# Kernel tuning notes

Hardware: AMD Instinct MI355X
Metric: run time of the kernel (lower is better)

Reference implementation:

```python
import jax, jax.numpy as jnp
import numpy as np

FC = 2048      # fc_feat_size
VEMB = 512     # video_embedding_size
WEMB = 512     # word_embedding_size
H = 512        # lstm_hidden_size
A = 256        # att_hidden_size
TV = 32        # video_time_step
TC = 20        # caption_time_step
BC = 16        # batch_size_caption
RP = 32        # rp_num (proposals per caption)
B = BC * RP    # batch_size
GLOVE = 300


def setup_inputs() -> dict:
    key = jax.random.key(0)
    ks = jax.random.split(key, 12)
    def u(k, shape):
        return jax.random.uniform(k, shape, jnp.float32, -0.1, 0.1)
    def n(k, shape, s=0.05):
        return jax.random.normal(k, shape, jnp.float32) * s
    return {
        "video_fc_feat": jax.random.normal(ks[0], (B, TV, FC), jnp.float32),
        "video_caption": jax.random.normal(ks[1], (BC, TC, GLOVE), jnp.float32),
        "cap_length_list": jax.random.randint(ks[2], (BC,), 0, TC),
        # video_embedding / word_embedding (Linear layers)
        "W_vemb": u(ks[3], (VEMB, FC)), "b_vemb": jnp.zeros((VEMB,), jnp.float32),
        "W_wemb": u(ks[4], (WEMB, GLOVE)), "b_wemb": jnp.zeros((WEMB,), jnp.float32),
        # LSTMCell for video (gate order i,f,g,o as in torch)
        "Wih_v": n(ks[5], (4 * H, VEMB)), "Whh_v": n(ks[6], (4 * H, H)),
        "bih_v": jnp.zeros((4 * H,), jnp.float32), "bhh_v": jnp.zeros((4 * H,), jnp.float32),
        # LSTMCell for caption
        "Wih_c": n(ks[7], (4 * H, WEMB)), "Whh_c": n(ks[8], (4 * H, H)),
        "bih_c": jnp.zeros((4 * H,), jnp.float32), "bhh_c": jnp.zeros((4 * H,), jnp.float32),
        # attention linears
        "W_vid": u(ks[9], (A, H)), "b_vid": jnp.zeros((A,), jnp.float32),
        "W_sen": u(ks[10], (A, H)), "b_sen": jnp.zeros((A,), jnp.float32),
        "W_att": u(ks[11], (1, A)), "b_att": jnp.zeros((1,), jnp.float32),
    }


def _lstm(x_seq, Wih, Whh, bih, bhh):
    # x_seq: [B, T, D] -> hidden states [B, T, H]; torch LSTMCell gate order i,f,g,o
    Bb = x_seq.shape[0]
    Hh = Whh.shape[1]
    def step(carry, x):
        h, c = carry
        g = x @ Wih.T + bih + h @ Whh.T + bhh
        i, f, gg, o = jnp.split(g, 4, axis=-1)
        c = jax.nn.sigmoid(f) * c + jax.nn.sigmoid(i) * jnp.tanh(gg)
        h = jax.nn.sigmoid(o) * jnp.tanh(c)
        return (h, c), h
    init = (jnp.zeros((Bb, Hh), x_seq.dtype), jnp.zeros((Bb, Hh), x_seq.dtype))
    _, hs = jax.lax.scan(step, init, jnp.swapaxes(x_seq, 0, 1))
    return jnp.swapaxes(hs, 0, 1)


def reference(video_fc_feat, video_caption, cap_length_list,
              W_vemb, b_vemb, W_wemb, b_wemb,
              Wih_v, Whh_v, bih_v, bhh_v,
              Wih_c, Whh_c, bih_c, bhh_c,
              W_vid, b_vid, W_sen, b_sen, W_att, b_att):
    Bb, TVv, _ = video_fc_feat.shape
    BCc, TCc, _ = video_caption.shape
    rp = Bb // BCc
    Hh = Whh_v.shape[1]

    # caption LSTM over embedded GloVe words
    cap_x = video_caption @ W_wemb.T + b_wemb                 # [BC, TC, WEMB]
    cap_h = _lstm(cap_x, Wih_c, Whh_c, bih_c, bhh_c)          # [BC, TC, H]
    # video LSTM over embedded fc features
    vid_x = video_fc_feat @ W_vemb.T + b_vemb                 # [B, TV, VEMB]
    vid_h = _lstm(vid_x, Wih_v, Whh_v, bih_v, bhh_v)          # [B, TV, H]

    # additive attention: tanh(vid_linear(h_v) + sen_linear(h_c)) -> att_linear
    c_lin = cap_h @ W_sen.T + b_sen                           # [BC, TC, A]
    v_lin = (vid_h @ W_vid.T + b_vid).reshape(BCc, rp, TVv, -1)  # [BC, RP, TV, A]
    scores = (jnp.tanh(v_lin[:, :, :, None, :] + c_lin[:, None, None, :, :])
              @ W_att.T + b_att)[..., 0]                      # [BC, RP, TV, TC]

    # ragged masked softmax over caption length (max(len, 1) as in original)
    cap_len = jnp.maximum(cap_length_list, 1)
    mask = jnp.arange(TCc)[None, :] < cap_len[:, None]        # [BC, TC]
    m = mask[:, None, None, :]
    w = jax.nn.softmax(jnp.where(m, scores, -1e9), axis=-1)
    w = jnp.where(m, w, 0.0)                                  # [BC, RP, TV, TC]

    att_cap = jnp.einsum('brvt,bth->brvh', w, cap_h)          # [BC, RP, TV, H]
    cap_ftr_mean = att_cap.mean(axis=2)                       # mean over video steps
    vid_mean = vid_h.mean(axis=1).reshape(BCc, rp, Hh)
    return (vid_mean, cap_ftr_mean)
```

## Files before the change

### kernel.cpp

```cpp
#include <hip/hip_runtime.h>
#include <hip/hip_bf16.h>

#define FCD 2048
#define VEMBD 512
#define WEMBD 512
#define HD 512
#define AD 256
#define TVD 32
#define TCD 20
#define BCD 16
#define RPD 32
#define BD 512
#define GLOVED 300

typedef __attribute__((ext_vector_type(8))) short short8v;
typedef __attribute__((ext_vector_type(4))) float f32x4;

__device__ __forceinline__ float sigf(float x) { return 1.0f / (1.0f + __expf(-x)); }
__device__ __forceinline__ float tanhfast(float x) {
    float e = __expf(2.0f * x);
    return 1.0f - 2.0f / (e + 1.0f);
}
__device__ __forceinline__ unsigned short f2bf(float x) {
    union { __hip_bfloat16 h; unsigned short u; } v;
    v.h = __float2bfloat16(x);
    return v.u;
}
__device__ __forceinline__ float b2f(unsigned short u) {
    union { unsigned int i; float f; } v;
    v.i = ((unsigned int)u) << 16;
    return v.f;
}

__launch_bounds__(256)
__global__ void conv_f2b_kernel(const float* __restrict__ src,
                                unsigned short* __restrict__ dst, int n4) {
    for (int i = blockIdx.x * 256 + threadIdx.x; i < n4; i += gridDim.x * 256) {
        const float4 v = ((const float4*)src)[i];
        ushort4 o;
        o.x = f2bf(v.x); o.y = f2bf(v.y); o.z = f2bf(v.z); o.w = f2bf(v.w);
        ((ushort4*)dst)[i] = o;
    }
}

__launch_bounds__(256)
__global__ void conv_wcat_perm_kernel(const float* __restrict__ Wih,
                                      const float* __restrict__ Whh,
                                      unsigned short* __restrict__ Wcat) {
    const int gp = blockIdx.x;
    const int q = (gp >> 4) & 3;
    const int hc = (gp >> 6) * 16 + (gp & 15);
    const long g = (long)(q * 512 + hc);
    for (int k = threadIdx.x; k < 512; k += 256) {
        Wcat[(long)gp * 1024 + k]       = f2bf(Wih[g * 512 + k]);
        Wcat[(long)gp * 1024 + 512 + k] = f2bf(Whh[g * 512 + k]);
    }
}

__launch_bounds__(256)
__global__ void conv_bsum_kernel(const float* __restrict__ bih,
                                 const float* __restrict__ bhh,
                                 float* __restrict__ bsum) {
    const int gp = blockIdx.x * 256 + threadIdx.x;
    if (gp < 2048) {
        const int q = (gp >> 4) & 3;
        const int hc = (gp >> 6) * 16 + (gp & 15);
        const int g = q * 512 + hc;
        bsum[gp] = bih[g] + bhh[g];
    }
}

template<int AF32, int OBF>
__launch_bounds__(256)
__global__ void mfma_gemm128(const void* __restrict__ A,
                             const unsigned short* __restrict__ Bw,
                             const float* __restrict__ bias,
                             void* __restrict__ Cout,
                             int M, int N, int K)
{
    __shared__ unsigned short As[128][72];
    __shared__ unsigned short Bs[128][72];
    const int m0 = blockIdx.x * 128;
    const int n0 = blockIdx.y * 128;
    const int tid = threadIdx.x;
    const int lane = tid & 63;
    const int wid = tid >> 6;
    const int wm = (wid >> 1) * 64;
    const int wn = (wid & 1) * 64;
    const int lrow = lane & 15;
    const int lko = (lane >> 4) * 8;
    const int sr = tid >> 1;
    const int sc = (tid & 1) * 32;

    f32x4 acc[4][4] = {};

    const float* Arow_f = (const float*)A + (long)(m0 + sr) * K;
    const unsigned short* Arow_b = (const unsigned short*)A + (long)(m0 + sr) * K;
    const unsigned short* Brow = Bw + (long)(n0 + sr) * K;

    if (AF32) {
#pragma unroll
        for (int i = 0; i < 8; i++) {
            const float4 v = *(const float4*)(Arow_f + sc + i * 4);
            unsigned short* d = &As[sr][sc + i * 4];
            d[0] = f2bf(v.x); d[1] = f2bf(v.y); d[2] = f2bf(v.z); d[3] = f2bf(v.w);
        }
    } else {
#pragma unroll
        for (int i = 0; i < 4; i++)
            *(short8v*)&As[sr][sc + i * 8] = *(const short8v*)(Arow_b + sc + i * 8);
    }
#pragma unroll
    for (int i = 0; i < 4; i++)
        *(short8v*)&Bs[sr][sc + i * 8] = *(const short8v*)(Brow + sc + i * 8);
    __syncthreads();

    const int nc = K >> 6;
    float4 paf[8];
    short8v pab[4], pb[4];
    for (int c = 0; c < nc; c++) {
        if (c < nc - 1) {
            const int k0 = (c + 1) * 64;
            if (AF32) {
#pragma unroll
                for (int i = 0; i < 8; i++)
                    paf[i] = *(const float4*)(Arow_f + k0 + sc + i * 4);
            } else {
#pragma unroll
                for (int i = 0; i < 4; i++)
                    pab[i] = *(const short8v*)(Arow_b + k0 + sc + i * 8);
            }
#pragma unroll
            for (int i = 0; i < 4; i++)
                pb[i] = *(const short8v*)(Brow + k0 + sc + i * 8);
        }
#pragma unroll
        for (int kk = 0; kk < 2; kk++) {
            short8v a[4], b[4];
#pragma unroll
            for (int mi = 0; mi < 4; mi++)
                a[mi] = *(const short8v*)&As[wm + mi * 16 + lrow][kk * 32 + lko];
#pragma unroll
            for (int ni = 0; ni < 4; ni++)
                b[ni] = *(const short8v*)&Bs[wn + ni * 16 + lrow][kk * 32 + lko];
#pragma unroll
            for (int mi = 0; mi < 4; mi++)
#pragma unroll
                for (int ni = 0; ni < 4; ni++)
                    acc[mi][ni] = __builtin_amdgcn_mfma_f32_16x16x32_bf16(
                        a[mi], b[ni], acc[mi][ni], 0, 0, 0);
        }
        __syncthreads();
        if (c < nc - 1) {
            if (AF32) {
#pragma unroll
                for (int i = 0; i < 8; i++) {
                    unsigned short* d = &As[sr][sc + i * 4];
                    d[0] = f2bf(paf[i].x); d[1] = f2bf(paf[i].y);
                    d[2] = f2bf(paf[i].z); d[3] = f2bf(paf[i].w);
                }
            } else {
#pragma unroll
                for (int i = 0; i < 4; i++)
                    *(short8v*)&As[sr][sc + i * 8] = pab[i];
            }
#pragma unroll
            for (int i = 0; i < 4; i++)
                *(short8v*)&Bs[sr][sc + i * 8] = pb[i];
            __syncthreads();
        }
    }

    const int rbase = (lane >> 4) * 4;
#pragma unroll
    for (int ni = 0; ni < 4; ni++) {
        const int col = n0 + wn + ni * 16 + lrow;
        const float bv = bias[col];
#pragma unroll
        for (int mi = 0; mi < 4; mi++) {
#pragma unroll
            for (int j = 0; j < 4; j++) {
                const long row = m0 + wm + mi * 16 + rbase + j;
                const float val = acc[mi][ni][j] + bv;
                if (OBF) ((unsigned short*)Cout)[row * N + col] = f2bf(val);
                else     ((float*)Cout)[row * N + col] = val;
            }
        }
    }
}

__launch_bounds__(256, 2)
__global__ void step_fused(const unsigned short* __restrict__ vx,
                           const unsigned short* __restrict__ h_in,
                           unsigned short* __restrict__ h_out,
                           const unsigned short* __restrict__ Wcat,
                           const float* __restrict__ bsum,
                           float* __restrict__ c_state,
                           unsigned short* __restrict__ vid_h,
                           int t,
                           const float* __restrict__ xg,
                           const float* __restrict__ Whh_c,
                           const float* __restrict__ bhh_c,
                           const float* __restrict__ hc_in,
                           float* __restrict__ hc_out,
                           float* __restrict__ cap_cst,
                           float* __restrict__ cap_h)
{
    __shared__ __align__(16) unsigned char smem[26112];
    const int bx = blockIdx.x;
    const int tid = threadIdx.x;

    if (bx >= 512) {
        const int h0 = (bx - 512) * 16;
        float* Wsc = (float*)smem;
        float* Hshc = (float*)(smem + 17408);
        const int tx = tid & 15;
        const int ty = tid >> 4;
        const int lrow2 = tid >> 2;
        const int lq = tid & 3;
        float acc4[4] = {};

        for (int k0 = 0; k0 < 512; k0 += 64) {
            {
                const int q = lrow2 >> 4;
                const int hcc = lrow2 & 15;
                const float* src = Whh_c + (long)(q * 512 + h0 + hcc) * 512 + k0 + lq * 16;
                const int col = hcc * 4 + q;
#pragma unroll
                for (int j = 0; j < 4; j++) {
                    const float4 v = *(const float4*)(src + j * 4);
                    Wsc[(lq * 16 + j * 4 + 0) * 68 + col] = v.x;
                    Wsc[(lq * 16 + j * 4 + 1) * 68 + col] = v.y;
                    Wsc[(lq * 16 + j * 4 + 2) * 68 + col] = v.z;
                    Wsc[(lq * 16 + j * 4 + 3) * 68 + col] = v.w;
                }
            }
            {
                const int lb = tid >> 4;
                const int lk4 = (tid & 15) * 4;
                *(float4*)&Hshc[lb * 68 + lk4] = *(const float4*)(hc_in + (long)lb * 512 + k0 + lk4);
            }
            __syncthreads();
#pragma unroll
            for (int kq = 0; kq < 16; kq++) {
                const float4 h4 = *(const float4*)&Hshc[ty * 68 + kq * 4];
                const float4 w0 = *(const float4*)&Wsc[(kq * 4 + 0) * 68 + tx * 4];
                const float4 w1 = *(const float4*)&Wsc[(kq * 4 + 1) * 68 + tx * 4];
                const float4 w2 = *(const float4*)&Wsc[(kq * 4 + 2) * 68 + tx * 4];
                const float4 w3 = *(const float4*)&Wsc[(kq * 4 + 3) * 68 + tx * 4];
                acc4[0] += h4.x * w0.x + h4.y * w1.x + h4.z * w2.x + h4.w * w3.x;
                acc4[1] += h4.x * w0.y + h4.y * w1.y + h4.z * w2.y + h4.w * w3.y;
                acc4[2] += h4.x * w0.z + h4.y * w1.z + h4.z * w2.z + h4.w * w3.z;
                acc4[3] += h4.x * w0.w + h4.y * w1.w + h4.z * w2.w + h4.w * w3.w;
            }
            __syncthreads();
        }
        const int hc = h0 + tx;
        const long xrow = (long)(ty * TCD + t) * 2048;
        const float gi = acc4[0] + xg[xrow + hc]        + bhh_c[hc];
        const float gf = acc4[1] + xg[xrow + 512 + hc]  + bhh_c[512 + hc];
        const float gg = acc4[2] + xg[xrow + 1024 + hc] + bhh_c[1024 + hc];
        const float go = acc4[3] + xg[xrow + 1536 + hc] + bhh_c[1536 + hc];
        const float c_old = cap_cst[(long)ty * 512 + hc];
        const float ii = sigf(gi), ff = sigf(gf), g2 = tanhfast(gg), oo = sigf(go);
        const float c = ff * c_old + ii * g2;
        const float h = oo * tanhfast(c);
        cap_cst[(long)ty * 512 + hc] = c;
        hc_out[(long)ty * 512 + hc] = h;
        cap_h[(long)(ty * TCD + t) * 512 + hc] = h;
        return;
    }

    const int n0 = (bx & 31) * 64;
    const int b0 = (bx >> 5) * 32;
    const int lane = tid & 63;
    const int w = tid >> 6;
    const int bi = w & 1;
    const int nq = w >> 1;
    const int lrow = lane & 15;
    const int lko = (lane >> 4) * 8;
    const int sra = tid >> 3;
    const int sca = (tid & 7) * 16;

    unsigned short* As = (unsigned short*)smem;
    unsigned short* Ws = (unsigned short*)(smem + 8704);

    const unsigned short* arow_vx = vx + ((long)(b0 + sra) * TVD + t) * 512;
    const unsigned short* arow_h  = h_in + (long)(b0 + sra) * 512;
    const unsigned short* wrow0   = Wcat + (long)(n0 + sra) * 1024;
    const unsigned short* wrow1   = Wcat + (long)(n0 + sra + 32) * 1024;

    f32x4 acc[2] = {};

    *(short8v*)&As[sra * 136 + sca]     = *(const short8v*)(arow_vx + sca);
    *(short8v*)&As[sra * 136 + sca + 8] = *(const short8v*)(arow_vx + sca + 8);
    *(short8v*)&Ws[sra * 136 + sca]            = *(const short8v*)(wrow0 + sca);
    *(short8v*)&Ws[sra * 136 + sca + 8]        = *(const short8v*)(wrow0 + sca + 8);
    *(short8v*)&Ws[(sra + 32) * 136 + sca]     = *(const short8v*)(wrow1 + sca);
    *(short8v*)&Ws[(sra + 32) * 136 + sca + 8] = *(const short8v*)(wrow1 + sca + 8);
    __syncthreads();

    short8v pa0, pa1, pw0, pw1, pw2, pw3;
    for (int c = 0; c < 8; c++) {
        if (c < 7) {
            const int k0 = (c + 1) * 128;
            const unsigned short* ap = (k0 < 512) ? (arow_vx + k0) : (arow_h + (k0 - 512));
            pa0 = *(const short8v*)(ap + sca);
            pa1 = *(const short8v*)(ap + sca + 8);
            pw0 = *(const short8v*)(wrow0 + k0 + sca);
            pw1 = *(const short8v*)(wrow0 + k0 + sca + 8);
            pw2 = *(const short8v*)(wrow1 + k0 + sca);
            pw3 = *(const short8v*)(wrow1 + k0 + sca + 8);
        }
#pragma unroll
        for (int kk = 0; kk < 4; kk++) {
            const short8v a = *(const short8v*)&As[(bi * 16 + lrow) * 136 + kk * 32 + lko];
#pragma unroll
            for (int nl = 0; nl < 2; nl++) {
                const short8v b = *(const short8v*)&Ws[((nq * 2 + nl) * 16 + lrow) * 136 + kk * 32 + lko];
                acc[nl] = __builtin_amdgcn_mfma_f32_16x16x32_bf16(a, b, acc[nl], 0, 0, 0);
            }
        }
        __syncthreads();
        if (c < 7) {
            *(short8v*)&As[sra * 136 + sca]            = pa0;
            *(short8v*)&As[sra * 136 + sca + 8]        = pa1;
            *(short8v*)&Ws[sra * 136 + sca]            = pw0;
            *(short8v*)&Ws[sra * 136 + sca + 8]        = pw1;
            *(short8v*)&Ws[(sra + 32) * 136 + sca]     = pw2;
            *(short8v*)&Ws[(sra + 32) * 136 + sca + 8] = pw3;
            __syncthreads();
        }
    }

    float* red = (float*)smem;
    const int rbase = (lane >> 4) * 4;
    if (w >= 2) {
#pragma unroll
        for (int nl = 0; nl < 2; nl++)
#pragma unroll
            for (int j = 0; j < 4; j++)
                red[nl * 512 + (bi * 16 + rbase + j) * 16 + lrow] = acc[nl][j];
    }
    __syncthreads();
    if (w < 2) {
        const int hc = (n0 >> 2) + lrow;
        const float bs0 = bsum[n0 + lrow];
        const float bs1 = bsum[n0 + 16 + lrow];
        const float bs2 = bsum[n0 + 32 + lrow];
        const float bs3 = bsum[n0 + 48 + lrow];
#pragma unroll
        for (int j = 0; j < 4; j++) {
            const int blocal = bi * 16 + rbase + j;
            const long b = b0 + blocal;
            const float gi = acc[0][j] + bs0;
            const float gf = acc[1][j] + bs1;
            const float gg = red[blocal * 16 + lrow] + bs2;
            const float go = red[512 + blocal * 16 + lrow] + bs3;
            const float c_old = c_state[b * 512 + hc];
            const float ii = sigf(gi), ff = sigf(gf), g2 = tanhfast(gg), oo = sigf(go);
            const float cn = ff * c_old + ii * g2;
            const float h = oo * tanhfast(cn);
            c_state[b * 512 + hc] = cn;
            h_out[b * 512 + hc] = f2bf(h);
            vid_h[(b * TVD + t) * 512 + hc] = f2bf(h);
        }
    }
}

__launch_bounds__(256)
__global__ void gemm_bias_kernel(const float* __restrict__ A,
                                 const float* __restrict__ Bw,
                                 const float* __restrict__ bias,
                                 float* __restrict__ C,
                                 int M, int N, int K) {
    __shared__ float As[16][68];
    __shared__ float Bs[16][68];
    const int n0 = blockIdx.x * 64;
    const int m0 = blockIdx.y * 64;
    const int tid = threadIdx.x;
    const int tx = tid & 15;
    const int ty = tid >> 4;
    const int lrow = tid >> 2;
    const int lk4 = (tid & 3) * 4;

    float acc[4][4] = {};

    for (int k0 = 0; k0 < K; k0 += 16) {
        {
            const float* src = A + (long)(m0 + lrow) * K + k0 + lk4;
            float4 v;
            if (k0 + 16 <= K) v = *(const float4*)src;
            else {
                v.x = (k0 + lk4 + 0 < K) ? src[0] : 0.f;
                v.y = (k0 + lk4 + 1 < K) ? src[1] : 0.f;
                v.z = (k0 + lk4 + 2 < K) ? src[2] : 0.f;
                v.w = (k0 + lk4 + 3 < K) ? src[3] : 0.f;
            }
            As[lk4 + 0][lrow] = v.x; As[lk4 + 1][lrow] = v.y;
            As[lk4 + 2][lrow] = v.z; As[lk4 + 3][lrow] = v.w;
        }
        {
            const float* src = Bw + (long)(n0 + lrow) * K + k0 + lk4;
            float4 v;
            if (k0 + 16 <= K) v = *(const float4*)src;
            else {
                v.x = (k0 + lk4 + 0 < K) ? src[0] : 0.f;
                v.y = (k0 + lk4 + 1 < K) ? src[1] : 0.f;
                v.z = (k0 + lk4 + 2 < K) ? src[2] : 0.f;
                v.w = (k0 + lk4 + 3 < K) ? src[3] : 0.f;
            }
            Bs[lk4 + 0][lrow] = v.x; Bs[lk4 + 1][lrow] = v.y;
            Bs[lk4 + 2][lrow] = v.z; Bs[lk4 + 3][lrow] = v.w;
        }
        __syncthreads();
#pragma unroll
        for (int kk = 0; kk < 16; kk++) {
            const float4 av = *(const float4*)&As[kk][ty * 4];
            const float4 bv = *(const float4*)&Bs[kk][tx * 4];
            acc[0][0] += av.x * bv.x; acc[0][1] += av.x * bv.y; acc[0][2] += av.x * bv.z; acc[0][3] += av.x * bv.w;
            acc[1][0] += av.y * bv.x; acc[1][1] += av.y * bv.y; acc[1][2] += av.y * bv.z; acc[1][3] += av.y * bv.w;
            acc[2][0] += av.z * bv.x; acc[2][1] += av.z * bv.y; acc[2][2] += av.z * bv.z; acc[2][3] += av.z * bv.w;
            acc[3][0] += av.w * bv.x; acc[3][1] += av.w * bv.y; acc[3][2] += av.w * bv.z; acc[3][3] += av.w * bv.w;
        }
        __syncthreads();
    }

    const float b0v = bias[n0 + tx * 4 + 0];
    const float b1v = bias[n0 + tx * 4 + 1];
    const float b2v = bias[n0 + tx * 4 + 2];
    const float b3v = bias[n0 + tx * 4 + 3];
#pragma unroll
    for (int i = 0; i < 4; i++) {
        float* dst = C + (long)(m0 + ty * 4 + i) * N + n0 + tx * 4;
        dst[0] = acc[i][0] + b0v;
        dst[1] = acc[i][1] + b1v;
        dst[2] = acc[i][2] + b2v;
        dst[3] = acc[i][3] + b3v;
    }
}

__launch_bounds__(256)
__global__ void attn_kernel(const float* __restrict__ v_lin,
                            const float* __restrict__ c_lin,
                            const float* __restrict__ W_att,
                            const float* __restrict__ b_att,
                            const int* __restrict__ cap_len,
                            const float* __restrict__ cap_h,
                            float* __restrict__ out2)
{
    const int br = blockIdx.x;
    const int bc = br >> 5;
    const int tid = threadIdx.x;
    const int lane = tid & 63;
    const int wv = tid >> 6;
    __shared__ float cl[TCD][AD];
    __shared__ float vl[AD];
    __shared__ float sl[TVD][TCD];
    __shared__ float wsum[TCD];

    for (int tt = 0; tt < TCD; tt++)
        cl[tt][tid] = c_lin[(long)(bc * TCD + tt) * AD + tid];
    const float wa0 = W_att[lane];
    const float wa1 = W_att[64 + lane];
    const float wa2 = W_att[128 + lane];
    const float wa3 = W_att[192 + lane];
    const float batt = b_att[0];
    __syncthreads();

    for (int v = 0; v < TVD; v++) {
        vl[tid] = v_lin[((long)br * TVD + v) * AD + tid];
        __syncthreads();
        const float v0 = vl[lane], v1 = vl[64 + lane], v2 = vl[128 + lane], v3 = vl[192 + lane];
#pragma unroll
        for (int dt = 0; dt < 5; dt++) {
            const int t = wv * 5 + dt;
            float s = tanhfast(v0 + cl[t][lane]) * wa0
                    + tanhfast(v1 + cl[t][64 + lane]) * wa1
                    + tanhfast(v2 + cl[t][128 + lane]) * wa2
                    + tanhfast(v3 + cl[t][192 + lane]) * wa3;
            for (int off = 32; off > 0; off >>= 1) s += __shfl_down(s, off, 64);
            if (lane == 0) sl[v][t] = s + batt;
        }
        __syncthreads();
    }

    int L = cap_len[bc];
    if (L < 1) L = 1;
    if (tid < TVD) {
        const int v = tid;
        float m = -1e30f;
        for (int t = 0; t < TCD; t++)
            if (t < L) m = fmaxf(m, sl[v][t]);
        float sum = 0.f;
        for (int t = 0; t < TCD; t++)
            if (t < L) sum += __expf(sl[v][t] - m);
        const float inv = 1.f / sum;
        for (int t = 0; t < TCD; t++)
            sl[v][t] = (t < L) ? __expf(sl[v][t] - m) * inv : 0.f;
    }
    __syncthreads();
    if (tid < TCD) {
        float s = 0.f;
        for (int v = 0; v < TVD; v++) s += sl[v][tid];
        wsum[tid] = s * (1.0f / TVD);
    }
    __syncthreads();

    const float* chb = cap_h + (long)bc * TCD * HD;
#pragma unroll
    for (int r = 0; r < 2; r++) {
        const int h = r * 256 + tid;
        float s = 0.f;
#pragma unroll
        for (int t = 0; t < TCD; t++)
            s += wsum[t] * chb[t * HD + h];
        out2[(long)br * HD + h] = s;
    }
}

__launch_bounds__(256)
__global__ void vidmean_bf_kernel(const unsigned short* __restrict__ vid_h,
                                  float* __restrict__ out1)
{
    const int idx = blockIdx.x * 256 + threadIdx.x;
    const int b = idx >> 6;
    const int h8 = (idx & 63) * 8;
    float s[8] = {};
    for (int t = 0; t < TVD; t++) {
        const short8v v = *(const short8v*)(vid_h + ((long)b * TVD + t) * 512 + h8);
#pragma unroll
        for (int j = 0; j < 8; j++) s[j] += b2f((unsigned short)v[j]);
    }
#pragma unroll
    for (int j = 0; j < 8; j++)
        out1[(long)b * 512 + h8 + j] = s[j] * (1.0f / TVD);
}

extern "C" void kernel_launch(void* const* d_in, const int* in_sizes, int n_in,
                              void* d_out, int out_size, void* d_ws, size_t ws_size,
                              hipStream_t stream) {
    const float* video_fc      = (const float*)d_in[0];
    const float* video_caption = (const float*)d_in[1];
    const int*   cap_len       = (const int*)d_in[2];
    const float* W_vemb = (const float*)d_in[3];
    const float* b_vemb = (const float*)d_in[4];
    const float* W_wemb = (const float*)d_in[5];
    const float* b_wemb = (const float*)d_in[6];
    const float* Wih_v  = (const float*)d_in[7];
    const float* Whh_v  = (const float*)d_in[8];
    const float* bih_v  = (const float*)d_in[9];
    const float* bhh_v  = (const float*)d_in[10];
    const float* Wih_c  = (const float*)d_in[11];
    const float* Whh_c  = (const float*)d_in[12];
    const float* bih_c  = (const float*)d_in[13];
    const float* bhh_c  = (const float*)d_in[14];
    const float* W_vid  = (const float*)d_in[15];
    const float* b_vid  = (const float*)d_in[16];
    const float* W_sen  = (const float*)d_in[17];
    const float* b_sen  = (const float*)d_in[18];
    const float* W_att  = (const float*)d_in[19];
    const float* b_att  = (const float*)d_in[20];

    float* out1 = (float*)d_out;
    float* out2 = out1 + BD * HD;

    float* ws = (float*)d_ws;
    size_t off = 0;
    auto alloc = [&](size_t nfloats) {
        float* p = ws + off;
        off += (nfloats + 63) & ~(size_t)63;
        return p;
    };
    unsigned short* vidx_bf = (unsigned short*)alloc((size_t)BD * TVD * VEMBD / 2);
    unsigned short* vidh_bf = (unsigned short*)alloc((size_t)BD * TVD * HD / 2);
    unsigned short* h_bf_a  = (unsigned short*)alloc((size_t)BD * HD / 2);
    unsigned short* h_bf_b  = (unsigned short*)alloc((size_t)BD * HD / 2);
    float* c_st    = alloc((size_t)BD * HD);
    float* v_lin   = alloc((size_t)BD * TVD * AD);
    unsigned short* Wvemb_bf = (unsigned short*)alloc((size_t)VEMBD * FCD / 2);
    unsigned short* Wvid_bf  = (unsigned short*)alloc((size_t)AD * HD / 2);
    unsigned short* Wcat_bf  = (unsigned short*)alloc((size_t)2048 * 1024 / 2);
    float* bsum    = alloc(2048);
    float* cap_x   = alloc((size_t)BCD * TCD * WEMBD);
    float* xg_c    = alloc((size_t)BCD * TCD * 4 * HD);
    float* cap_h   = alloc((size_t)BCD * TCD * HD);
    float* c_lin   = alloc((size_t)BCD * TCD * AD);
    float* cap_ha  = alloc((size_t)BCD * HD);
    float* cap_hb  = alloc((size_t)BCD * HD);
    float* cap_cst = alloc((size_t)BCD * HD);
    const size_t fcn = (size_t)BD * TVD * FCD;
    const bool preconv = ((off + fcn / 2 + 64) * sizeof(float) <= ws_size);
    unsigned short* vidfc_bf = preconv ? (unsigned short*)alloc(fcn / 2) : nullptr;

    hipMemsetAsync(h_bf_a, 0, (size_t)BD * HD * sizeof(unsigned short), stream);
    hipMemsetAsync(c_st, 0, (size_t)BD * HD * sizeof(float), stream);
    hipMemsetAsync(cap_ha, 0, (size_t)BCD * HD * sizeof(float), stream);
    hipMemsetAsync(cap_cst, 0, (size_t)BCD * HD * sizeof(float), stream);

    conv_f2b_kernel<<<512, 256, 0, stream>>>(W_vemb, Wvemb_bf, VEMBD * FCD / 4);
    conv_f2b_kernel<<<128, 256, 0, stream>>>(W_vid, Wvid_bf, AD * HD / 4);
    conv_wcat_perm_kernel<<<2048, 256, 0, stream>>>(Wih_v, Whh_v, Wcat_bf);
    conv_bsum_kernel<<<8, 256, 0, stream>>>(bih_v, bhh_v, bsum);

    gemm_bias_kernel<<<dim3(WEMBD / 64, (BCD * TCD) / 64), 256, 0, stream>>>(
        video_caption, W_wemb, b_wemb, cap_x, BCD * TCD, WEMBD, GLOVED);
    gemm_bias_kernel<<<dim3((4 * HD) / 64, (BCD * TCD) / 64), 256, 0, stream>>>(
        cap_x, Wih_c, bih_c, xg_c, BCD * TCD, 4 * HD, WEMBD);

    if (preconv) {
        conv_f2b_kernel<<<2048, 256, 0, stream>>>(video_fc, vidfc_bf, (int)(fcn / 4));
        mfma_gemm128<0, 1><<<dim3((BD * TVD) / 128, VEMBD / 128), 256, 0, stream>>>(
            vidfc_bf, Wvemb_bf, b_vemb, vidx_bf, BD * TVD, VEMBD, FCD);
    } else {
        mfma_gemm128<1, 1><<<dim3((BD * TVD) / 128, VEMBD / 128), 256, 0, stream>>>(
            video_fc, Wvemb_bf, b_vemb, vidx_bf, BD * TVD, VEMBD, FCD);
    }

    for (int t = 0; t < TVD; t++) {
        const unsigned short* hin = (t & 1) ? h_bf_b : h_bf_a;
        unsigned short* hout = (t & 1) ? h_bf_a : h_bf_b;
        const float* chin = (t & 1) ? cap_hb : cap_ha;
        float* chout = (t & 1) ? cap_ha : cap_hb;
        const int nblk = (t < TCD) ? 544 : 512;
        step_fused<<<nblk, 256, 0, stream>>>(
            vidx_bf, hin, hout, Wcat_bf, bsum, c_st, vidh_bf, t,
            xg_c, Whh_c, bhh_c, chin, chout, cap_cst, cap_h);
    }

    gemm_bias_kernel<<<dim3(AD / 64, (BCD * TCD) / 64), 256, 0, stream>>>(
        cap_h, W_sen, b_sen, c_lin, BCD * TCD, AD, HD);
    mfma_gemm128<0, 0><<<dim3((BD * TVD) / 128, AD / 128), 256, 0, stream>>>(
        vidh_bf, Wvid_bf, b_vid, v_lin, BD * TVD, AD, HD);

    attn_kernel<<<BD, 256, 0, stream>>>(v_lin, c_lin, W_att, b_att, cap_len, cap_h, out2);
    vidmean_bf_kernel<<<(BD * HD / 8) / 256, 256, 0, stream>>>(vidh_bf, out1);
}
```

Baseline: 847.5 us.

## Double K-chunk size in fused LSTM step and restructure attention scoring

The fused LSTM step kernel now stages 256-wide K chunks instead of 128, halving the number of barrier-separated load/compute iterations, and raises the occupancy hint to 3 blocks per CU despite nearly doubling shared memory. The attention kernel preloads all video-linear rows and W_att into padded shared memory and has each thread compute full 256-wide dot products for one video step and up to three caption steps, removing the per-step warp shuffle reductions and the two barriers per video step. This trades more shared memory and registers for fewer syncs and reductions, and could lower occupancy.

```diff
diff --git a/kernel.cpp b/kernel.cpp
--- a/kernel.cpp
+++ b/kernel.cpp
@@ -189,7 +189,7 @@
     }
 }
 
-__launch_bounds__(256, 2)
+__launch_bounds__(256, 3)
 __global__ void step_fused(const unsigned short* __restrict__ vx,
                            const unsigned short* __restrict__ h_in,
                            unsigned short* __restrict__ h_out,
@@ -206,7 +206,7 @@
                            float* __restrict__ cap_cst,
                            float* __restrict__ cap_h)
 {
-    __shared__ __align__(16) unsigned char smem[26112];
+    __shared__ __align__(16) unsigned char smem[50688];
     const int bx = blockIdx.x;
     const int tid = threadIdx.x;
 
@@ -280,55 +280,56 @@
     const int lrow = lane & 15;
     const int lko = (lane >> 4) * 8;
     const int sra = tid >> 3;
-    const int sca = (tid & 7) * 16;
+    const int sca = (tid & 7) * 32;
+    const int srw = tid >> 2;
+    const int scw = (tid & 3) * 64;
 
     unsigned short* As = (unsigned short*)smem;
-    unsigned short* Ws = (unsigned short*)(smem + 8704);
+    unsigned short* Ws = (unsigned short*)(smem + 16896);
 
     const unsigned short* arow_vx = vx + ((long)(b0 + sra) * TVD + t) * 512;
     const unsigned short* arow_h  = h_in + (long)(b0 + sra) * 512;
-    const unsigned short* wrow0   = Wcat + (long)(n0 + sra) * 1024;
-    const unsigned short* wrow1   = Wcat + (long)(n0 + sra + 32) * 1024;
+    const unsigned short* wrowp   = Wcat + (long)(n0 + srw) * 1024;
 
     f32x4 acc[2] = {};
 
-    *(short8v*)&As[sra * 136 + sca]     = *(const short8v*)(arow_vx + sca);
-    *(short8v*)&As[sra * 136 + sca + 8] = *(const short8v*)(arow_vx + sca + 8);
-    *(short8v*)&Ws[sra * 136 + sca]            = *(const short8v*)(wrow0 + sca);
-    *(short8v*)&Ws[sra * 136 + sca + 8]        = *(const short8v*)(wrow0 + sca + 8);
-    *(short8v*)&Ws[(sra + 32) * 136 + sca]     = *(const short8v*)(wrow1 + sca);
-    *(short8v*)&Ws[(sra + 32) * 136 + sca + 8] = *(const short8v*)(wrow1 + sca + 8);
+#pragma unroll
+    for (int i = 0; i < 4; i++)
+        *(short8v*)&As[sra * 264 + sca + i * 8] = *(const short8v*)(arow_vx + sca + i * 8);
+#pragma unroll
+    for (int i = 0; i < 8; i++)
+        *(short8v*)&Ws[srw * 264 + scw + i * 8] = *(const short8v*)(wrowp + scw + i * 8);
     __syncthreads();
 
-    short8v pa0, pa1, pw0, pw1, pw2, pw3;
-    for (int c = 0; c < 8; c++) {
-        if (c < 7) {
-            const int k0 = (c + 1) * 128;
+    short8v pa[4], pw[8];
+    for (int c = 0; c < 4; c++) {
+        if (c < 3) {
+            const int k0 = (c + 1) * 256;
             const unsigned short* ap = (k0 < 512) ? (arow_vx + k0) : (arow_h + (k0 - 512));
-            pa0 = *(const short8v*)(ap + sca);
-            pa1 = *(const short8v*)(ap + sca + 8);
-            pw0 = *(const short8v*)(wrow0 + k0 + sca);
-            pw1 = *(const short8v*)(wrow0 + k0 + sca + 8);
-            pw2 = *(const short8v*)(wrow1 + k0 + sca);
-            pw3 = *(const short8v*)(wrow1 + k0 + sca + 8);
-        }
-#pragma unroll
-        for (int kk = 0; kk < 4; kk++) {
-            const short8v a = *(const short8v*)&As[(bi * 16 + lrow) * 136 + kk * 32 + lko];
+#pragma unroll
+            for (int i = 0; i < 4; i++)
+                pa[i] = *(const short8v*)(ap + sca + i * 8);
+#pragma unroll
+            for (int i = 0; i < 8; i++)
+                pw[i] = *(const short8v*)(wrowp + k0 + scw + i * 8);
+        }
+#pragma unroll
+        for (int kk = 0; kk < 8; kk++) {
+            const short8v a = *(const short8v*)&As[(bi * 16 + lrow) * 264 + kk * 32 + lko];
 #pragma unroll
             for (int nl = 0; nl < 2; nl++) {
-                const short8v b = *(const short8v*)&Ws[((nq * 2 + nl) * 16 + lrow) * 136 + kk * 32 + lko];
+                const short8v b = *(const short8v*)&Ws[((nq * 2 + nl) * 16 + lrow) * 264 + kk * 32 + lko];
                 acc[nl] = __builtin_amdgcn_mfma_f32_16x16x32_bf16(a, b, acc[nl], 0, 0, 0);
             }
         }
         __syncthreads();
-        if (c < 7) {
-            *(short8v*)&As[sra * 136 + sca]            = pa0;
-            *(short8v*)&As[sra * 136 + sca + 8]        = pa1;
-            *(short8v*)&Ws[sra * 136 + sca]            = pw0;
-            *(short8v*)&Ws[sra * 136 + sca + 8]        = pw1;
-            *(short8v*)&Ws[(sra + 32) * 136 + sca]     = pw2;
-            *(short8v*)&Ws[(sra + 32) * 136 + sca + 8] = pw3;
+        if (c < 3) {
+#pragma unroll
+            for (int i = 0; i < 4; i++)
+                *(short8v*)&As[sra * 264 + sca + i * 8] = pa[i];
+#pragma unroll
+            for (int i = 0; i < 8; i++)
+                *(short8v*)&Ws[srw * 264 + scw + i * 8] = pw[i];
             __syncthreads();
         }
     }
@@ -440,7 +441,8 @@
     }
 }
 
-__launch_bounds__(256)
+#define PFL 258
+__launch_bounds__(256, 2)
 __global__ void attn_kernel(const float* __restrict__ v_lin,
                             const float* __restrict__ c_lin,
                             const float* __restrict__ W_att,
@@ -452,38 +454,51 @@
     const int br = blockIdx.x;
     const int bc = br >> 5;
     const int tid = threadIdx.x;
-    const int lane = tid & 63;
-    const int wv = tid >> 6;
-    __shared__ float cl[TCD][AD];
-    __shared__ float vl[AD];
+    __shared__ float cl[TCD][PFL];
+    __shared__ float vl[TVD][PFL];
+    __shared__ float wa[AD];
     __shared__ float sl[TVD][TCD];
     __shared__ float wsum[TCD];
 
-    for (int tt = 0; tt < TCD; tt++)
-        cl[tt][tid] = c_lin[(long)(bc * TCD + tt) * AD + tid];
-    const float wa0 = W_att[lane];
-    const float wa1 = W_att[64 + lane];
-    const float wa2 = W_att[128 + lane];
-    const float wa3 = W_att[192 + lane];
+    {
+        const float* csrc = c_lin + (long)bc * TCD * AD;
+        for (int idx = tid; idx < TCD * 128; idx += 256) {
+            const int row = idx >> 7, c2 = (idx & 127) * 2;
+            *(float2*)&cl[row][c2] = *(const float2*)(csrc + row * AD + c2);
+        }
+        const float* vsrc = v_lin + (long)br * TVD * AD;
+        for (int idx = tid; idx < TVD * 128; idx += 256) {
+            const int row = idx >> 7, c2 = (idx & 127) * 2;
+            *(float2*)&vl[row][c2] = *(const float2*)(vsrc + row * AD + c2);
+        }
+        wa[tid] = W_att[tid];
+    }
     const float batt = b_att[0];
     __syncthreads();
 
-    for (int v = 0; v < TVD; v++) {
-        vl[tid] = v_lin[((long)br * TVD + v) * AD + tid];
-        __syncthreads();
-        const float v0 = vl[lane], v1 = vl[64 + lane], v2 = vl[128 + lane], v3 = vl[192 + lane];
-#pragma unroll
-        for (int dt = 0; dt < 5; dt++) {
-            const int t = wv * 5 + dt;
-            float s = tanhfast(v0 + cl[t][lane]) * wa0
-                    + tanhfast(v1 + cl[t][64 + lane]) * wa1
-                    + tanhfast(v2 + cl[t][128 + lane]) * wa2
-                    + tanhfast(v3 + cl[t][192 + lane]) * wa3;
-            for (int off = 32; off > 0; off >>= 1) s += __shfl_down(s, off, 64);
-            if (lane == 0) sl[v][t] = s + batt;
-        }
-        __syncthreads();
-    }
+    {
+        const int v = tid & 31;
+        const int tg = tid >> 5;
+        const int t0 = tg, t1 = tg + 8, t2 = tg + 16;
+        const bool ok2 = (t2 < TCD);
+        const int t2c = ok2 ? t2 : 0;
+        float s0 = 0.f, s1 = 0.f, s2 = 0.f;
+#pragma unroll 4
+        for (int i = 0; i < 128; i++) {
+            const float2 w2 = *(const float2*)&wa[2 * i];
+            const float2 vv = *(const float2*)&vl[v][2 * i];
+            const float2 c0 = *(const float2*)&cl[t0][2 * i];
+            const float2 c1 = *(const float2*)&cl[t1][2 * i];
+            const float2 c2 = *(const float2*)&cl[t2c][2 * i];
+            s0 += tanhfast(vv.x + c0.x) * w2.x + tanhfast(vv.y + c0.y) * w2.y;
+            s1 += tanhfast(vv.x + c1.x) * w2.x + tanhfast(vv.y + c1.y) * w2.y;
+            s2 += tanhfast(vv.x + c2.x) * w2.x + tanhfast(vv.y + c2.y) * w2.y;
+        }
+        sl[v][t0] = s0 + batt;
+        sl[v][t1] = s1 + batt;
+        if (ok2) sl[v][t2] = s2 + batt;
+    }
+    __syncthreads();
 
     int L = cap_len[bc];
     if (L < 1) L = 1;
```

After: 980.9 us. 1.16x slower.

## Restructure attention scoring to per-thread (v,t) dot products with all v_lin staged

Applied to the files above, without the earlier changes.

Loads all 32 v_lin rows and the c_lin tile into padded shared memory at once. Each thread then computes full 256-wide scores for one video step and up to three caption steps, instead of running one wave-level shuffle reduction per (v,t) pair. This removes 32 iterations of per-v barriers and the cross-lane reductions, and asks the compiler for two blocks per CU. In exchange shared memory use grows and the scheduler gets less latency hiding.

```diff
diff --git a/kernel.cpp b/kernel.cpp
--- a/kernel.cpp
+++ b/kernel.cpp
@@ -440,7 +440,8 @@
     }
 }
 
-__launch_bounds__(256)
+#define PFL 258
+__launch_bounds__(256, 2)
 __global__ void attn_kernel(const float* __restrict__ v_lin,
                             const float* __restrict__ c_lin,
                             const float* __restrict__ W_att,
@@ -452,38 +453,51 @@
     const int br = blockIdx.x;
     const int bc = br >> 5;
     const int tid = threadIdx.x;
-    const int lane = tid & 63;
-    const int wv = tid >> 6;
-    __shared__ float cl[TCD][AD];
-    __shared__ float vl[AD];
+    __shared__ float cl[TCD][PFL];
+    __shared__ float vl[TVD][PFL];
+    __shared__ float wa[AD];
     __shared__ float sl[TVD][TCD];
     __shared__ float wsum[TCD];
 
-    for (int tt = 0; tt < TCD; tt++)
-        cl[tt][tid] = c_lin[(long)(bc * TCD + tt) * AD + tid];
-    const float wa0 = W_att[lane];
-    const float wa1 = W_att[64 + lane];
-    const float wa2 = W_att[128 + lane];
-    const float wa3 = W_att[192 + lane];
+    {
+        const float* csrc = c_lin + (long)bc * TCD * AD;
+        for (int idx = tid; idx < TCD * 128; idx += 256) {
+            const int row = idx >> 7, c2 = (idx & 127) * 2;
+            *(float2*)&cl[row][c2] = *(const float2*)(csrc + row * AD + c2);
+        }
+        const float* vsrc = v_lin + (long)br * TVD * AD;
+        for (int idx = tid; idx < TVD * 128; idx += 256) {
+            const int row = idx >> 7, c2 = (idx & 127) * 2;
+            *(float2*)&vl[row][c2] = *(const float2*)(vsrc + row * AD + c2);
+        }
+        wa[tid] = W_att[tid];
+    }
     const float batt = b_att[0];
     __syncthreads();
 
-    for (int v = 0; v < TVD; v++) {
-        vl[tid] = v_lin[((long)br * TVD + v) * AD + tid];
-        __syncthreads();
-        const float v0 = vl[lane], v1 = vl[64 + lane], v2 = vl[128 + lane], v3 = vl[192 + lane];
-#pragma unroll
-        for (int dt = 0; dt < 5; dt++) {
-            const int t = wv * 5 + dt;
-            float s = tanhfast(v0 + cl[t][lane]) * wa0
-                    + tanhfast(v1 + cl[t][64 + lane]) * wa1
-                    + tanhfast(v2 + cl[t][128 + lane]) * wa2
-                    + tanhfast(v3 + cl[t][192 + lane]) * wa3;
-            for (int off = 32; off > 0; off >>= 1) s += __shfl_down(s, off, 64);
-            if (lane == 0) sl[v][t] = s + batt;
-        }
-        __syncthreads();
-    }
+    {
+        const int v = tid & 31;
+        const int tg = tid >> 5;
+        const int t0 = tg, t1 = tg + 8, t2 = tg + 16;
+        const bool ok2 = (t2 < TCD);
+        const int t2c = ok2 ? t2 : 0;
+        float s0 = 0.f, s1 = 0.f, s2 = 0.f;
+#pragma unroll 4
+        for (int i = 0; i < 128; i++) {
+            const float2 w2 = *(const float2*)&wa[2 * i];
+            const float2 vv = *(const float2*)&vl[v][2 * i];
+            const float2 c0 = *(const float2*)&cl[t0][2 * i];
+            const float2 c1 = *(const float2*)&cl[t1][2 * i];
+            const float2 c2 = *(const float2*)&cl[t2c][2 * i];
+            s0 += tanhfast(vv.x + c0.x) * w2.x + tanhfast(vv.y + c0.y) * w2.y;
+            s1 += tanhfast(vv.x + c1.x) * w2.x + tanhfast(vv.y + c1.y) * w2.y;
+            s2 += tanhfast(vv.x + c2.x) * w2.x + tanhfast(vv.y + c2.y) * w2.y;
+        }
+        sl[v][t0] = s0 + batt;
+        sl[v][t1] = s1 + batt;
+        if (ok2) sl[v][t2] = s2 + batt;
+    }
+    __syncthreads();
 
     int L = cap_len[bc];
     if (L < 1) L = 1;
```

New measurement: 818.7 us (median of 2 runs). -3.4%, faster.
